# Kernel optimization log

Hardware: AMD Instinct MI355X
Metric: run time of the kernel (lower is better)

Reference implementation:

```python
import jax, jax.numpy as jnp
import numpy as np
import math

DIM_IN = 768
RED = 256
FS = 384


def setup_inputs() -> dict:
    key = jax.random.key(0)
    ks = jax.random.split(key, 20)
    B, Nq, Nk = 16, 1024, FS
    inp = {
        "query_feature": jax.random.normal(ks[0], (B, Nq, DIM_IN), jnp.float32),
        "Input_feature": jax.random.normal(ks[1], (B, Nk, DIM_IN), jnp.float32),
    }
    # six q/k projections: Linear(dim_in -> reduce_dim), torch weight layout [out,in]
    names = ["q1", "q2", "q3", "k1", "k2", "k3"]
    for i, n in enumerate(names):
        inp[f"W{n}"] = 0.01 * jax.random.normal(ks[2 + i], (RED, DIM_IN), jnp.float32)
        inp[f"b{n}"] = jnp.zeros((RED,), jnp.float32)
    # self.layer: Linear(Fs_size -> 1)
    inp["layer_w"] = 0.01 * jax.random.normal(ks[10], (1, FS), jnp.float32)
    inp["layer_b"] = jnp.zeros((1,), jnp.float32)
    # output_layer: Linear(2*dim_in -> dim_in)
    inp["Wout"] = 0.01 * jax.random.normal(ks[11], (DIM_IN, 2 * DIM_IN), jnp.float32)
    inp["bout"] = jnp.zeros((DIM_IN,), jnp.float32)
    return inp


def _proj_center(x, W, b):
    # Linear then subtract per-feature mean over the token axis (dim=1)
    y = jnp.einsum("bnd,rd->bnr", x, W) + b
    return y - y.mean(axis=1, keepdims=True)


def reference(query_feature, Input_feature,
              Wq1, bq1, Wq2, bq2, Wq3, bq3,
              Wk1, bk1, Wk2, bk2, Wk3, bk3,
              layer_w, layer_b, Wout, bout):
    scale = 1.0 / math.sqrt(RED)
    q1 = _proj_center(query_feature, Wq1, bq1)
    q2 = _proj_center(query_feature, Wq2, bq2)
    q3 = _proj_center(query_feature, Wq3, bq3)
    k1 = _proj_center(Input_feature, Wk1, bk1)
    k2 = _proj_center(Input_feature, Wk2, bk2)
    k3 = _proj_center(Input_feature, Wk3, bk3)

    aw1 = jax.nn.softmax(jnp.einsum("bnr,bmr->bnm", q1, q2) * scale, axis=2)  # [B,Nq,Nq]
    aw2 = jax.nn.softmax(jnp.einsum("bnr,bmr->bnm", k1, k2) * scale, axis=2)  # [B,Nk,Nk]
    aw3 = jax.nn.softmax(jnp.einsum("bnr,bmr->bnm", q3, k3) * scale, axis=2)  # [B,Nq,Nk]

    attention_feature1 = jnp.einsum("bnm,bmd->bnd", aw1, query_feature)  # [B,Nq,D]
    hidden = jnp.einsum("bnm,om->bno", aw2, layer_w) + layer_b  # [B,Nk,1]
    hidden = jax.nn.softmax(hidden, axis=1)
    add = aw3 + jnp.swapaxes(hidden, 1, 2)  # broadcast [B,1,Nk]
    attention_feature2 = jnp.einsum("bnm,bmd->bnd", add, Input_feature)  # [B,Nq,D]

    cat = jnp.concatenate([attention_feature1, attention_feature2], axis=2)  # [B,Nq,2D]
    out = jnp.einsum("bnc,dc->bnd", cat, Wout) + bout
    return (cat, out)
```

## Files before the change

### kernel.cpp

```cpp
#include <hip/hip_runtime.h>

#define BATCH 16
#define NQ 1024
#define NK 384
#define DIM 768
#define RED 256
#define CATD 1536

typedef __attribute__((ext_vector_type(4))) float f32x4;
typedef __attribute__((ext_vector_type(8))) short short8;

__device__ __forceinline__ short f2bf(float f) {
    unsigned u = __builtin_bit_cast(unsigned, f);
    u = (u + 0x7FFF + ((u >> 16) & 1)) >> 16;
    return (short)u;
}

#define GLOAD_LDS16(g, l) __builtin_amdgcn_global_load_lds( \
    (const __attribute__((address_space(1))) unsigned int*)(g), \
    (__attribute__((address_space(3))) unsigned int*)(l), 16, 0, 0)

struct GemmDesc {
    const short* A; const short* B;
    float* Cf; short* Cb; const float* bias;
    int K, lda, ldb, ldcf, ldcb;
    long sA, sB, sCf, sCb;
    float scale;
    int nx, ny;
    int start;
};

__global__ __launch_bounds__(256) void gemm_routed(
    GemmDesc d0, GemmDesc d1, GemmDesc d2, int nseg)
{
    __shared__ short Asl[2][128 * 64];
    __shared__ short Bsl[2][128 * 64];

    unsigned lin = blockIdx.x;
    const unsigned nwg = gridDim.x;
    const unsigned qc = nwg >> 3, rc = nwg & 7;
    const unsigned xcd = lin & 7, pos = lin >> 3;
    unsigned nid = (xcd < rc ? xcd * (qc + 1) : rc * (qc + 1) + (xcd - rc) * qc) + pos;

    GemmDesc d = d0;
    if (nseg > 1 && nid >= (unsigned)d1.start) d = d1;
    if (nseg > 2 && nid >= (unsigned)d2.start) d = d2;

    unsigned r = nid - (unsigned)d.start;
    const unsigned bx = r % (unsigned)d.nx; r /= (unsigned)d.nx;
    const unsigned by = r % (unsigned)d.ny;
    const unsigned bz = r / (unsigned)d.ny;

    const short* Ab = d.A + (long)bz * d.sA;
    const short* Bb = d.B + (long)bz * d.sB;
    const int m0 = by * 128, n0 = bx * 128;
    const int tid = threadIdx.x;
    const int lane = tid & 63, wid = tid >> 6;
    const int am0 = (wid >> 1) * 64, bn0 = (wid & 1) * 64;
    const int lr = lane & 15, lg = lane >> 4;
    const int lda = d.lda, ldb = d.ldb;

    f32x4 acc[4][4] = {};

    auto stage = [&](int buf, int k0) {
        #pragma unroll
        for (int i = 0; i < 4; i++) {
            int e = (tid + i * 256) * 8;
            int rr = e >> 6, c = e & 63;
            GLOAD_LDS16(Ab + (long)(m0 + rr) * lda + k0 + c, &Asl[buf][e]);
        }
        #pragma unroll
        for (int i = 0; i < 4; i++) {
            int e = (tid + i * 256) * 8;
            int rr = e >> 6, c = e & 63;
            GLOAD_LDS16(Bb + (long)(n0 + rr) * ldb + k0 + c, &Bsl[buf][e]);
        }
    };
    auto compute = [&](int buf) {
        #pragma unroll
        for (int ks = 0; ks < 2; ks++) {
            short8 af[4], bfv[4];
            #pragma unroll
            for (int m = 0; m < 4; m++)
                af[m] = *(const short8*)&Asl[buf][(am0 + m * 16 + lr) * 64 + ks * 32 + lg * 8];
            #pragma unroll
            for (int n = 0; n < 4; n++)
                bfv[n] = *(const short8*)&Bsl[buf][(bn0 + n * 16 + lr) * 64 + ks * 32 + lg * 8];
            #pragma unroll
            for (int m = 0; m < 4; m++)
                #pragma unroll
                for (int n = 0; n < 4; n++)
                    acc[m][n] = __builtin_amdgcn_mfma_f32_16x16x32_bf16(
                        af[m], bfv[n], acc[m][n], 0, 0, 0);
        }
    };

    const int nt = d.K >> 6;
    stage(0, 0);
    __syncthreads();
    int cur = 0;
    for (int t = 0; t < nt; ++t) {
        if (t + 1 < nt) stage(cur ^ 1, (t + 1) << 6);
        compute(cur);
        if (t + 1 < nt) { __syncthreads(); cur ^= 1; }
    }

    const float scale = d.scale;
    float* Cfb = d.Cf ? d.Cf + (long)bz * d.sCf : nullptr;
    short* Cbb = d.Cb ? d.Cb + (long)bz * d.sCb : nullptr;
    if (Cfb && Cbb) {
        #pragma unroll
        for (int m = 0; m < 4; m++)
            #pragma unroll
            for (int n = 0; n < 4; n++) {
                int col = n0 + bn0 + n * 16 + lr;
                #pragma unroll
                for (int j = 0; j < 4; j++) {
                    long row = m0 + am0 + m * 16 + lg * 4 + j;
                    float v = acc[m][n][j] * scale;
                    Cfb[row * d.ldcf + col] = v;
                    Cbb[row * d.ldcb + col] = f2bf(v);
                }
            }
    } else if (Cfb) {
        const float* bias = d.bias;
        #pragma unroll
        for (int m = 0; m < 4; m++)
            #pragma unroll
            for (int n = 0; n < 4; n++) {
                int col = n0 + bn0 + n * 16 + lr;
                float bv = bias ? bias[col] : 0.f;
                #pragma unroll
                for (int j = 0; j < 4; j++) {
                    long row = m0 + am0 + m * 16 + lg * 4 + j;
                    Cfb[row * d.ldcf + col] = acc[m][n][j] * scale + bv;
                }
            }
    } else {
        #pragma unroll
        for (int m = 0; m < 4; m++)
            #pragma unroll
            for (int n = 0; n < 4; n++) {
                int col = n0 + bn0 + n * 16 + lr;
                #pragma unroll
                for (int j = 0; j < 4; j++) {
                    long row = m0 + am0 + m * 16 + lg * 4 + j;
                    Cbb[row * d.ldcb + col] = f2bf(acc[m][n][j] * scale);
                }
            }
    }
}

__global__ __launch_bounds__(256) void colsum(
    const float* __restrict__ X, float* __restrict__ mean, int N, int chunk)
{
    int b = blockIdx.x;
    int dd = blockIdx.y * 256 + threadIdx.x;
    int n0 = blockIdx.z * chunk;
    float s = 0.f;
    for (int n = n0; n < n0 + chunk; n++)
        s += X[((long)b * N + n) * DIM + dd];
    atomicAdd(&mean[b * DIM + dd], s);
}

template<int N>
__global__ __launch_bounds__(256) void prep_input(
    const float* __restrict__ X, const float* __restrict__ mean,
    short* __restrict__ Xc, short* __restrict__ XT, float invN)
{
    __shared__ short tile[32][33];
    int b = blockIdx.z;
    int n0 = blockIdx.x * 32, d0 = blockIdx.y * 32;
    int tx = threadIdx.x & 31, ty = threadIdx.x >> 5;
    const float* Xb = X + (long)b * N * DIM;
    short* Xcb = Xc + (long)b * N * DIM;
    float mv = mean[b * DIM + d0 + tx] * invN;
    #pragma unroll
    for (int i = 0; i < 4; i++) {
        int n = n0 + ty + i * 8;
        float x = Xb[(long)n * DIM + d0 + tx];
        tile[ty + i * 8][tx] = f2bf(x);
        Xcb[(long)n * DIM + d0 + tx] = f2bf(x - mv);
    }
    __syncthreads();
    short* XTb = XT + (long)b * DIM * N;
    #pragma unroll
    for (int i = 0; i < 4; i++) {
        int dd = d0 + ty + i * 8;
        XTb[(long)dd * N + n0 + tx] = tile[tx][ty + i * 8];
    }
}

struct WP { const float* p[7]; };
__global__ __launch_bounds__(256) void cvt_weights(
    WP wp, short* __restrict__ Wqb, short* __restrict__ Wkb,
    short* __restrict__ WoutB)
{
    const int WSZ = RED * DIM / 8;
    const int OSZ = DIM * CATD / 8;
    int i = blockIdx.x * 256 + threadIdx.x;
    if (i >= 6 * WSZ + OSZ) return;
    const float* src;
    short* dst;
    if (i < 6 * WSZ) {
        int w = i / WSZ, o = i - w * WSZ;
        src = wp.p[w] + (long)o * 8;
        dst = (w < 3 ? Wqb + (long)w * RED * DIM
                     : Wkb + (long)(w - 3) * RED * DIM) + (long)o * 8;
    } else {
        int o = i - 6 * WSZ;
        src = wp.p[6] + (long)o * 8;
        dst = WoutB + (long)o * 8;
    }
    const f32x4* s = (const f32x4*)src;
    f32x4 x0 = s[0], x1 = s[1];
    short8 o8;
    o8[0] = f2bf(x0[0]); o8[1] = f2bf(x0[1]); o8[2] = f2bf(x0[2]); o8[3] = f2bf(x0[3]);
    o8[4] = f2bf(x1[0]); o8[5] = f2bf(x1[1]); o8[6] = f2bf(x1[2]); o8[7] = f2bf(x1[3]);
    *(short8*)dst = o8;
}

template<int L>
__device__ __forceinline__ void softmax_body(
    const float* __restrict__ p, short* __restrict__ po,
    const float* __restrict__ addv)
{
    const int tid = threadIdx.x;
    const int C = (L + 255) >> 8;
    float v[C];
    float mx = -3.0e38f;
    #pragma unroll
    for (int c = 0; c < C; c++) {
        int i = tid + c * 256;
        v[c] = (i < L) ? p[i] : -3.0e38f;
        mx = fmaxf(mx, v[c]);
    }
    __shared__ float rmax[4], rsum[4];
    #pragma unroll
    for (int o = 1; o < 64; o <<= 1) mx = fmaxf(mx, __shfl_xor(mx, o));
    if ((tid & 63) == 0) rmax[tid >> 6] = mx;
    __syncthreads();
    mx = fmaxf(fmaxf(rmax[0], rmax[1]), fmaxf(rmax[2], rmax[3]));
    float s = 0.f;
    #pragma unroll
    for (int c = 0; c < C; c++) {
        float e = __expf(v[c] - mx);
        v[c] = e;
        s += e;
    }
    #pragma unroll
    for (int o = 1; o < 64; o <<= 1) s += __shfl_xor(s, o);
    if ((tid & 63) == 0) rsum[tid >> 6] = s;
    __syncthreads();
    s = rsum[0] + rsum[1] + rsum[2] + rsum[3];
    float inv = 1.0f / s;
    if (addv) {
        #pragma unroll
        for (int c = 0; c < C; c++) {
            int i = tid + c * 256;
            if (i < L) po[i] = f2bf(v[c] * inv + addv[i]);
        }
    } else {
        #pragma unroll
        for (int c = 0; c < C; c++) {
            int i = tid + c * 256;
            if (i < L) po[i] = f2bf(v[c] * inv);
        }
    }
}

__global__ __launch_bounds__(256) void softmax_two(
    const float* __restrict__ S1, short* __restrict__ P1,
    const float* __restrict__ S3, short* __restrict__ P3,
    const float* __restrict__ hid)
{
    long row = blockIdx.x;
    if (row < (long)BATCH * NQ) {
        softmax_body<NQ>(S1 + row * NQ, P1 + row * NQ, nullptr);
    } else {
        row -= (long)BATCH * NQ;
        int b = (int)(row / NQ);
        softmax_body<NK>(S3 + row * NK, P3 + row * NK, hid + (long)b * NK);
    }
}

__global__ __launch_bounds__(256) void softmax_dot(
    const float* __restrict__ S2, const float* __restrict__ lw,
    float* __restrict__ scores)
{
    long row = blockIdx.x;
    const float* p = S2 + row * NK;
    const int tid = threadIdx.x;
    const int C = 2;
    float v[C];
    float mx = -3.0e38f;
    #pragma unroll
    for (int c = 0; c < C; c++) {
        int i = tid + c * 256;
        v[c] = (i < NK) ? p[i] : -3.0e38f;
        mx = fmaxf(mx, v[c]);
    }
    __shared__ float rmax[4], rsum[4], rdot[4];
    #pragma unroll
    for (int o = 1; o < 64; o <<= 1) mx = fmaxf(mx, __shfl_xor(mx, o));
    if ((tid & 63) == 0) rmax[tid >> 6] = mx;
    __syncthreads();
    mx = fmaxf(fmaxf(rmax[0], rmax[1]), fmaxf(rmax[2], rmax[3]));
    float s = 0.f, dt = 0.f;
    #pragma unroll
    for (int c = 0; c < C; c++) {
        int i = tid + c * 256;
        float e = __expf(v[c] - mx);
        s += e;
        dt += (i < NK) ? e * lw[i] : 0.f;
    }
    #pragma unroll
    for (int o = 1; o < 64; o <<= 1) { s += __shfl_xor(s, o); dt += __shfl_xor(dt, o); }
    if ((tid & 63) == 0) { rsum[tid >> 6] = s; rdot[tid >> 6] = dt; }
    __syncthreads();
    if (tid == 0) {
        s = rsum[0] + rsum[1] + rsum[2] + rsum[3];
        dt = rdot[0] + rdot[1] + rdot[2] + rdot[3];
        scores[row] = dt / s;
    }
}

__global__ __launch_bounds__(384) void hid_softmax(
    const float* __restrict__ scores, float* __restrict__ hid)
{
    int b = blockIdx.x;
    int n = threadIdx.x;
    float s = scores[b * NK + n];
    __shared__ float red[6];
    float mx = s;
    #pragma unroll
    for (int o = 1; o < 64; o <<= 1) mx = fmaxf(mx, __shfl_xor(mx, o));
    int wid = n >> 6;
    if ((n & 63) == 0) red[wid] = mx;
    __syncthreads();
    mx = red[0];
    #pragma unroll
    for (int w = 1; w < 6; w++) mx = fmaxf(mx, red[w]);
    float e = __expf(s - mx);
    float sm = e;
    #pragma unroll
    for (int o = 1; o < 64; o <<= 1) sm += __shfl_xor(sm, o);
    __syncthreads();
    if ((n & 63) == 0) red[wid] = sm;
    __syncthreads();
    sm = 0.f;
    #pragma unroll
    for (int w = 0; w < 6; w++) sm += red[w];
    hid[b * NK + n] = e / sm;
}

extern "C" void kernel_launch(void* const* d_in, const int* in_sizes, int n_in,
                              void* d_out, int out_size, void* d_ws, size_t ws_size,
                              hipStream_t stream)
{
    const float* Qf  = (const float*)d_in[0];
    const float* If  = (const float*)d_in[1];
    const float* lw  = (const float*)d_in[14];
    const float* bout= (const float*)d_in[17];

    float* cat = (float*)d_out;
    float* out = (float*)d_out + (long)BATCH * NQ * CATD;

    char* ws = (char*)d_ws;
    size_t off = 0;
    auto alloc = [&](size_t bytes) { char* p = ws + off; off += (bytes + 255) & ~(size_t)255; return p; };

    float* S1    = (float*)alloc((size_t)BATCH * NQ * NQ * 4);
    float* S2    = (float*)alloc((size_t)BATCH * NK * NK * 4);
    float* S3    = (float*)alloc((size_t)BATCH * NQ * NK * 4);
    short* Qc    = (short*)alloc((size_t)BATCH * NQ * DIM * 2);
    short* Kc    = (short*)alloc((size_t)BATCH * NK * DIM * 2);
    short* QfT   = (short*)alloc((size_t)BATCH * NQ * DIM * 2);
    short* IfT   = (short*)alloc((size_t)BATCH * NK * DIM * 2);
    short* q_all = (short*)alloc((size_t)BATCH * NQ * 3 * RED * 2);
    short* k_all = (short*)alloc((size_t)BATCH * NK * 3 * RED * 2);
    short* P1    = (short*)alloc((size_t)BATCH * NQ * NQ * 2);
    short* P3    = (short*)alloc((size_t)BATCH * NQ * NK * 2);
    short* catbf = (short*)alloc((size_t)BATCH * NQ * CATD * 2);
    short* Wqb   = (short*)alloc((size_t)3 * RED * DIM * 2);
    short* Wkb   = (short*)alloc((size_t)3 * RED * DIM * 2);
    short* WoutB = (short*)alloc((size_t)DIM * CATD * 2);
    float* means = (float*)alloc((size_t)2 * BATCH * DIM * 4);
    float* scores= (float*)alloc((size_t)BATCH * NK * 4);
    float* hid   = (float*)alloc((size_t)BATCH * NK * 4);

    float* meanQ = means;
    float* meanK = means + BATCH * DIM;

    hipMemsetAsync(means, 0, (size_t)2 * BATCH * DIM * 4, stream);

    colsum<<<dim3(BATCH, DIM / 256, NQ / 128), 256, 0, stream>>>(Qf, meanQ, NQ, 128);
    colsum<<<dim3(BATCH, DIM / 256, NK / 128), 256, 0, stream>>>(If, meanK, NK, 128);

    prep_input<NQ><<<dim3(NQ / 32, DIM / 32, BATCH), 256, 0, stream>>>(Qf, meanQ, Qc, QfT, 1.0f / NQ);
    prep_input<NK><<<dim3(NK / 32, DIM / 32, BATCH), 256, 0, stream>>>(If, meanK, Kc, IfT, 1.0f / NK);

    {
        WP wp;
        wp.p[0] = (const float*)d_in[2];
        wp.p[1] = (const float*)d_in[4];
        wp.p[2] = (const float*)d_in[6];
        wp.p[3] = (const float*)d_in[8];
        wp.p[4] = (const float*)d_in[10];
        wp.p[5] = (const float*)d_in[12];
        wp.p[6] = (const float*)d_in[16];
        int total = 6 * (RED * DIM / 8) + DIM * CATD / 8;
        cvt_weights<<<(total + 255) / 256, 256, 0, stream>>>(wp, Wqb, Wkb, WoutB);
    }

    const float scale = 0.0625f;
    const long sQ = (long)NQ * 3 * RED, sK = (long)NK * 3 * RED;
    GemmDesc z = {};

    {
        GemmDesc dq = z, dk = z;
        dq.A = Qc; dq.B = Wqb; dq.Cb = q_all;
        dq.K = DIM; dq.lda = DIM; dq.ldb = DIM; dq.ldcb = 3 * RED;
        dq.scale = 1.0f; dq.nx = 6; dq.ny = BATCH * NQ / 128; dq.start = 0;
        dk = dq; dk.A = Kc; dk.B = Wkb; dk.Cb = k_all;
        dk.ny = BATCH * NK / 128; dk.start = 6 * (BATCH * NQ / 128);
        int total = dk.start + 6 * (BATCH * NK / 128);
        gemm_routed<<<total, 256, 0, stream>>>(dq, dk, z, 2);
    }

    {
        GemmDesc a = z, b = z, c = z;
        a.A = q_all; a.B = q_all + RED; a.Cf = S1;
        a.K = RED; a.lda = 3 * RED; a.ldb = 3 * RED; a.ldcf = NQ;
        a.sA = sQ; a.sB = sQ; a.sCf = (long)NQ * NQ;
        a.scale = scale; a.nx = NQ / 128; a.ny = NQ / 128; a.start = 0;
        b.A = k_all; b.B = k_all + RED; b.Cf = S2;
        b.K = RED; b.lda = 3 * RED; b.ldb = 3 * RED; b.ldcf = NK;
        b.sA = sK; b.sB = sK; b.sCf = (long)NK * NK;
        b.scale = scale; b.nx = NK / 128; b.ny = NK / 128;
        b.start = a.nx * a.ny * BATCH;
        c.A = q_all + 2 * RED; c.B = k_all + 2 * RED; c.Cf = S3;
        c.K = RED; c.lda = 3 * RED; c.ldb = 3 * RED; c.ldcf = NK;
        c.sA = sQ; c.sB = sK; c.sCf = (long)NQ * NK;
        c.scale = scale; c.nx = NK / 128; c.ny = NQ / 128;
        c.start = b.start + b.nx * b.ny * BATCH;
        int total = c.start + c.nx * c.ny * BATCH;
        gemm_routed<<<total, 256, 0, stream>>>(a, b, c, 3);
    }

    softmax_dot<<<BATCH * NK, 256, 0, stream>>>(S2, lw, scores);
    hid_softmax<<<BATCH, NK, 0, stream>>>(scores, hid);
    softmax_two<<<2 * BATCH * NQ, 256, 0, stream>>>(S1, P1, S3, P3, hid);

    {
        GemmDesc p1 = z, p2 = z;
        p1.A = P1; p1.B = QfT; p1.Cf = cat; p1.Cb = catbf;
        p1.K = NQ; p1.lda = NQ; p1.ldb = NQ; p1.ldcf = CATD; p1.ldcb = CATD;
        p1.sA = (long)NQ * NQ; p1.sB = (long)DIM * NQ;
        p1.sCf = (long)NQ * CATD; p1.sCb = (long)NQ * CATD;
        p1.scale = 1.0f; p1.nx = DIM / 128; p1.ny = NQ / 128; p1.start = 0;
        p2 = p1;
        p2.A = P3; p2.B = IfT; p2.Cf = cat + DIM; p2.Cb = catbf + DIM;
        p2.K = NK; p2.lda = NK; p2.ldb = NK;
        p2.sA = (long)NQ * NK; p2.sB = (long)DIM * NK;
        p2.start = p1.nx * p1.ny * BATCH;
        int total = 2 * p1.nx * p1.ny * BATCH;
        gemm_routed<<<total, 256, 0, stream>>>(p1, p2, z, 2);
    }

    {
        GemmDesc f = z;
        f.A = catbf; f.B = WoutB; f.Cf = out; f.bias = bout;
        f.K = CATD; f.lda = CATD; f.ldb = CATD; f.ldcf = DIM;
        f.scale = 1.0f; f.nx = DIM / 128; f.ny = BATCH * NQ / 128; f.start = 0;
        gemm_routed<<<f.nx * f.ny, 256, 0, stream>>>(f, z, z, 1);
    }
}
```

Baseline: 666.7 us.

## Enlarge GEMM tiles to 256x256 with 512-thread blocks and bounds clamping

Replaces the 128x128-tile, 256-thread routed GEMM with a 256x256-tile, 512-thread variant in which each wave computes a 128x64 sub-tile. Row loads are clamped and stores are guarded so that dimensions like 384 that are not multiples of 256 still work. The three epilogue branches are merged into one path. The aim is more operand reuse per LDS byte and fewer workgroups. In exchange it needs 128KB of LDS per block and many more accumulator registers. Padded tiles on the 384-wide problems waste compute, and fewer, larger blocks may underfill the CUs on the small batched GEMMs.

```diff
diff --git a/kernel.cpp b/kernel.cpp
--- a/kernel.cpp
+++ b/kernel.cpp
@@ -23,18 +23,18 @@
 struct GemmDesc {
     const short* A; const short* B;
     float* Cf; short* Cb; const float* bias;
-    int K, lda, ldb, ldcf, ldcb;
+    int M, N, K, lda, ldb, ldcf, ldcb;
     long sA, sB, sCf, sCb;
     float scale;
     int nx, ny;
     int start;
 };
 
-__global__ __launch_bounds__(256) void gemm_routed(
+__global__ __launch_bounds__(512, 2) void gemm256(
     GemmDesc d0, GemmDesc d1, GemmDesc d2, int nseg)
 {
-    __shared__ short Asl[2][128 * 64];
-    __shared__ short Bsl[2][128 * 64];
+    __shared__ short Asl[2][256 * 64];
+    __shared__ short Bsl[2][256 * 64];
 
     unsigned lin = blockIdx.x;
     const unsigned nwg = gridDim.x;
@@ -53,41 +53,45 @@
 
     const short* Ab = d.A + (long)bz * d.sA;
     const short* Bb = d.B + (long)bz * d.sB;
-    const int m0 = by * 128, n0 = bx * 128;
+    const int m0 = by * 256, n0 = bx * 256;
+    const int M = d.M, N = d.N;
     const int tid = threadIdx.x;
     const int lane = tid & 63, wid = tid >> 6;
-    const int am0 = (wid >> 1) * 64, bn0 = (wid & 1) * 64;
+    const int wr = wid >> 2, wc = wid & 3;
+    const int am0 = wr * 128, bn0 = wc * 64;
     const int lr = lane & 15, lg = lane >> 4;
     const int lda = d.lda, ldb = d.ldb;
 
-    f32x4 acc[4][4] = {};
+    f32x4 acc[8][4] = {};
 
     auto stage = [&](int buf, int k0) {
         #pragma unroll
         for (int i = 0; i < 4; i++) {
-            int e = (tid + i * 256) * 8;
+            int e = (tid + i * 512) * 8;
             int rr = e >> 6, c = e & 63;
-            GLOAD_LDS16(Ab + (long)(m0 + rr) * lda + k0 + c, &Asl[buf][e]);
+            int ra = m0 + rr; if (ra > M - 1) ra = M - 1;
+            GLOAD_LDS16(Ab + (long)ra * lda + k0 + c, &Asl[buf][e]);
         }
         #pragma unroll
         for (int i = 0; i < 4; i++) {
-            int e = (tid + i * 256) * 8;
+            int e = (tid + i * 512) * 8;
             int rr = e >> 6, c = e & 63;
-            GLOAD_LDS16(Bb + (long)(n0 + rr) * ldb + k0 + c, &Bsl[buf][e]);
+            int rb = n0 + rr; if (rb > N - 1) rb = N - 1;
+            GLOAD_LDS16(Bb + (long)rb * ldb + k0 + c, &Bsl[buf][e]);
         }
     };
     auto compute = [&](int buf) {
         #pragma unroll
         for (int ks = 0; ks < 2; ks++) {
-            short8 af[4], bfv[4];
+            short8 af[8], bfv[4];
             #pragma unroll
-            for (int m = 0; m < 4; m++)
+            for (int m = 0; m < 8; m++)
                 af[m] = *(const short8*)&Asl[buf][(am0 + m * 16 + lr) * 64 + ks * 32 + lg * 8];
             #pragma unroll
             for (int n = 0; n < 4; n++)
                 bfv[n] = *(const short8*)&Bsl[buf][(bn0 + n * 16 + lr) * 64 + ks * 32 + lg * 8];
             #pragma unroll
-            for (int m = 0; m < 4; m++)
+            for (int m = 0; m < 8; m++)
                 #pragma unroll
                 for (int n = 0; n < 4; n++)
                     acc[m][n] = __builtin_amdgcn_mfma_f32_16x16x32_bf16(
@@ -102,52 +106,30 @@
     for (int t = 0; t < nt; ++t) {
         if (t + 1 < nt) stage(cur ^ 1, (t + 1) << 6);
         compute(cur);
-        if (t + 1 < nt) { __syncthreads(); cur ^= 1; }
+        __syncthreads();
+        cur ^= 1;
     }
 
     const float scale = d.scale;
     float* Cfb = d.Cf ? d.Cf + (long)bz * d.sCf : nullptr;
     short* Cbb = d.Cb ? d.Cb + (long)bz * d.sCb : nullptr;
-    if (Cfb && Cbb) {
-        #pragma unroll
-        for (int m = 0; m < 4; m++)
+    const float* bias = d.bias;
+    #pragma unroll
+    for (int m = 0; m < 8; m++) {
+        #pragma unroll
+        for (int n = 0; n < 4; n++) {
+            int col = n0 + bn0 + n * 16 + lr;
+            if (col >= N) continue;
+            float bv = bias ? bias[col] : 0.f;
             #pragma unroll
-            for (int n = 0; n < 4; n++) {
-                int col = n0 + bn0 + n * 16 + lr;
-                #pragma unroll
-                for (int j = 0; j < 4; j++) {
-                    long row = m0 + am0 + m * 16 + lg * 4 + j;
-                    float v = acc[m][n][j] * scale;
-                    Cfb[row * d.ldcf + col] = v;
-                    Cbb[row * d.ldcb + col] = f2bf(v);
-                }
+            for (int j = 0; j < 4; j++) {
+                int row = m0 + am0 + m * 16 + lg * 4 + j;
+                if (row >= M) continue;
+                float v = acc[m][n][j] * scale + bv;
+                if (Cfb) Cfb[(long)row * d.ldcf + col] = v;
+                if (Cbb) Cbb[(long)row * d.ldcb + col] = f2bf(v);
             }
-    } else if (Cfb) {
-        const float* bias = d.bias;
-        #pragma unroll
-        for (int m = 0; m < 4; m++)
-            #pragma unroll
-            for (int n = 0; n < 4; n++) {
-                int col = n0 + bn0 + n * 16 + lr;
-                float bv = bias ? bias[col] : 0.f;
-                #pragma unroll
-                for (int j = 0; j < 4; j++) {
-                    long row = m0 + am0 + m * 16 + lg * 4 + j;
-                    Cfb[row * d.ldcf + col] = acc[m][n][j] * scale + bv;
-                }
-            }
-    } else {
-        #pragma unroll
-        for (int m = 0; m < 4; m++)
-            #pragma unroll
-            for (int n = 0; n < 4; n++) {
-                int col = n0 + bn0 + n * 16 + lr;
-                #pragma unroll
-                for (int j = 0; j < 4; j++) {
-                    long row = m0 + am0 + m * 16 + lg * 4 + j;
-                    Cbb[row * d.ldcb + col] = f2bf(acc[m][n][j] * scale);
-                }
-            }
+        }
     }
 }
 
@@ -420,32 +402,37 @@
     {
         GemmDesc dq = z, dk = z;
         dq.A = Qc; dq.B = Wqb; dq.Cb = q_all;
-        dq.K = DIM; dq.lda = DIM; dq.ldb = DIM; dq.ldcb = 3 * RED;
-        dq.scale = 1.0f; dq.nx = 6; dq.ny = BATCH * NQ / 128; dq.start = 0;
+        dq.M = BATCH * NQ; dq.N = 3 * RED; dq.K = DIM;
+        dq.lda = DIM; dq.ldb = DIM; dq.ldcb = 3 * RED;
+        dq.scale = 1.0f; dq.nx = 3; dq.ny = BATCH * NQ / 256; dq.start = 0;
         dk = dq; dk.A = Kc; dk.B = Wkb; dk.Cb = k_all;
-        dk.ny = BATCH * NK / 128; dk.start = 6 * (BATCH * NQ / 128);
-        int total = dk.start + 6 * (BATCH * NK / 128);
-        gemm_routed<<<total, 256, 0, stream>>>(dq, dk, z, 2);
+        dk.M = BATCH * NK; dk.ny = BATCH * NK / 256;
+        dk.start = dq.nx * dq.ny;
+        int total = dk.start + dk.nx * dk.ny;
+        gemm256<<<total, 512, 0, stream>>>(dq, dk, z, 2);
     }
 
     {
         GemmDesc a = z, b = z, c = z;
         a.A = q_all; a.B = q_all + RED; a.Cf = S1;
-        a.K = RED; a.lda = 3 * RED; a.ldb = 3 * RED; a.ldcf = NQ;
+        a.M = NQ; a.N = NQ; a.K = RED;
+        a.lda = 3 * RED; a.ldb = 3 * RED; a.ldcf = NQ;
         a.sA = sQ; a.sB = sQ; a.sCf = (long)NQ * NQ;
-        a.scale = scale; a.nx = NQ / 128; a.ny = NQ / 128; a.start = 0;
+        a.scale = scale; a.nx = 4; a.ny = 4; a.start = 0;
         b.A = k_all; b.B = k_all + RED; b.Cf = S2;
-        b.K = RED; b.lda = 3 * RED; b.ldb = 3 * RED; b.ldcf = NK;
+        b.M = NK; b.N = NK; b.K = RED;
+        b.lda = 3 * RED; b.ldb = 3 * RED; b.ldcf = NK;
         b.sA = sK; b.sB = sK; b.sCf = (long)NK * NK;
-        b.scale = scale; b.nx = NK / 128; b.ny = NK / 128;
+        b.scale = scale; b.nx = 2; b.ny = 2;
         b.start = a.nx * a.ny * BATCH;
         c.A = q_all + 2 * RED; c.B = k_all + 2 * RED; c.Cf = S3;
-        c.K = RED; c.lda = 3 * RED; c.ldb = 3 * RED; c.ldcf = NK;
+        c.M = NQ; c.N = NK; c.K = RED;
+        c.lda = 3 * RED; c.ldb = 3 * RED; c.ldcf = NK;
         c.sA = sQ; c.sB = sK; c.sCf = (long)NQ * NK;
-        c.scale = scale; c.nx = NK / 128; c.ny = NQ / 128;
+        c.scale = scale; c.nx = 2; c.ny = 4;
         c.start = b.start + b.nx * b.ny * BATCH;
         int total = c.start + c.nx * c.ny * BATCH;
-        gemm_routed<<<total, 256, 0, stream>>>(a, b, c, 3);
+        gemm256<<<total, 512, 0, stream>>>(a, b, c, 3);
     }
 
     softmax_dot<<<BATCH * NK, 256, 0, stream>>>(S2, lw, scores);
@@ -455,24 +442,26 @@
     {
         GemmDesc p1 = z, p2 = z;
         p1.A = P1; p1.B = QfT; p1.Cf = cat; p1.Cb = catbf;
-        p1.K = NQ; p1.lda = NQ; p1.ldb = NQ; p1.ldcf = CATD; p1.ldcb = CATD;
+        p1.M = NQ; p1.N = DIM; p1.K = NQ;
+        p1.lda = NQ; p1.ldb = NQ; p1.ldcf = CATD; p1.ldcb = CATD;
         p1.sA = (long)NQ * NQ; p1.sB = (long)DIM * NQ;
         p1.sCf = (long)NQ * CATD; p1.sCb = (long)NQ * CATD;
-        p1.scale = 1.0f; p1.nx = DIM / 128; p1.ny = NQ / 128; p1.start = 0;
+        p1.scale = 1.0f; p1.nx = 3; p1.ny = 4; p1.start = 0;
         p2 = p1;
         p2.A = P3; p2.B = IfT; p2.Cf = cat + DIM; p2.Cb = catbf + DIM;
         p2.K = NK; p2.lda = NK; p2.ldb = NK;
         p2.sA = (long)NQ * NK; p2.sB = (long)DIM * NK;
         p2.start = p1.nx * p1.ny * BATCH;
         int total = 2 * p1.nx * p1.ny * BATCH;
-        gemm_routed<<<total, 256, 0, stream>>>(p1, p2, z, 2);
+        gemm256<<<total, 512, 0, stream>>>(p1, p2, z, 2);
     }
 
     {
         GemmDesc f = z;
         f.A = catbf; f.B = WoutB; f.Cf = out; f.bias = bout;
-        f.K = CATD; f.lda = CATD; f.ldb = CATD; f.ldcf = DIM;
-        f.scale = 1.0f; f.nx = DIM / 128; f.ny = BATCH * NQ / 128; f.start = 0;
-        gemm_routed<<<f.nx * f.ny, 256, 0, stream>>>(f, z, z, 1);
-    }
-}
+        f.M = BATCH * NQ; f.N = DIM; f.K = CATD;
+        f.lda = CATD; f.ldb = CATD; f.ldcf = DIM;
+        f.scale = 1.0f; f.nx = 3; f.ny = BATCH * NQ / 256; f.start = 0;
+        gemm256<<<f.nx * f.ny, 512, 0, stream>>>(f, z, z, 1);
+    }
+}
```

Result: slower. 760.3 us (+14.0%).

## Store attention scores as bf16 in place and single-buffer GEMM LDS

Applied to the files above, without the earlier changes.

Attention score matrices S1/S2/S3 are now written by the GEMM as bf16 rather than fp32. The softmax kernels read them as bf16 and overwrite them in place, which removes the separate P1/P3 buffers and halves score-matrix traffic. The GEMM also drops LDS double buffering for a single buffer with two barriers per k-step. That halves shared memory per block, which may raise occupancy, but it gives up overlap between loads and MFMA work. Rounding the scores to bf16 before softmax also loses some precision.

```diff
diff --git a/kernel.cpp b/kernel.cpp
--- a/kernel.cpp
+++ b/kernel.cpp
@@ -14,6 +14,10 @@
     unsigned u = __builtin_bit_cast(unsigned, f);
     u = (u + 0x7FFF + ((u >> 16) & 1)) >> 16;
     return (short)u;
+}
+__device__ __forceinline__ float bf2f(short s) {
+    unsigned u = ((unsigned)(unsigned short)s) << 16;
+    return __builtin_bit_cast(float, u);
 }
 
 #define GLOAD_LDS16(g, l) __builtin_amdgcn_global_load_lds( \
@@ -33,8 +37,8 @@
 __global__ __launch_bounds__(256) void gemm_routed(
     GemmDesc d0, GemmDesc d1, GemmDesc d2, int nseg)
 {
-    __shared__ short Asl[2][128 * 64];
-    __shared__ short Bsl[2][128 * 64];
+    __shared__ short Asl[128 * 64];
+    __shared__ short Bsl[128 * 64];
 
     unsigned lin = blockIdx.x;
     const unsigned nwg = gridDim.x;
@@ -62,30 +66,29 @@
 
     f32x4 acc[4][4] = {};
 
-    auto stage = [&](int buf, int k0) {
+    for (int k0 = 0; k0 < d.K; k0 += 64) {
         #pragma unroll
         for (int i = 0; i < 4; i++) {
             int e = (tid + i * 256) * 8;
             int rr = e >> 6, c = e & 63;
-            GLOAD_LDS16(Ab + (long)(m0 + rr) * lda + k0 + c, &Asl[buf][e]);
+            GLOAD_LDS16(Ab + (long)(m0 + rr) * lda + k0 + c, Asl + e);
         }
         #pragma unroll
         for (int i = 0; i < 4; i++) {
             int e = (tid + i * 256) * 8;
             int rr = e >> 6, c = e & 63;
-            GLOAD_LDS16(Bb + (long)(n0 + rr) * ldb + k0 + c, &Bsl[buf][e]);
+            GLOAD_LDS16(Bb + (long)(n0 + rr) * ldb + k0 + c, Bsl + e);
         }
-    };
-    auto compute = [&](int buf) {
+        __syncthreads();
         #pragma unroll
         for (int ks = 0; ks < 2; ks++) {
             short8 af[4], bfv[4];
             #pragma unroll
             for (int m = 0; m < 4; m++)
-                af[m] = *(const short8*)&Asl[buf][(am0 + m * 16 + lr) * 64 + ks * 32 + lg * 8];
+                af[m] = *(const short8*)&Asl[(am0 + m * 16 + lr) * 64 + ks * 32 + lg * 8];
             #pragma unroll
             for (int n = 0; n < 4; n++)
-                bfv[n] = *(const short8*)&Bsl[buf][(bn0 + n * 16 + lr) * 64 + ks * 32 + lg * 8];
+                bfv[n] = *(const short8*)&Bsl[(bn0 + n * 16 + lr) * 64 + ks * 32 + lg * 8];
             #pragma unroll
             for (int m = 0; m < 4; m++)
                 #pragma unroll
@@ -93,16 +96,7 @@
                     acc[m][n] = __builtin_amdgcn_mfma_f32_16x16x32_bf16(
                         af[m], bfv[n], acc[m][n], 0, 0, 0);
         }
-    };
-
-    const int nt = d.K >> 6;
-    stage(0, 0);
-    __syncthreads();
-    int cur = 0;
-    for (int t = 0; t < nt; ++t) {
-        if (t + 1 < nt) stage(cur ^ 1, (t + 1) << 6);
-        compute(cur);
-        if (t + 1 < nt) { __syncthreads(); cur ^= 1; }
+        __syncthreads();
     }
 
     const float scale = d.scale;
@@ -222,8 +216,7 @@
 
 template<int L>
 __device__ __forceinline__ void softmax_body(
-    const float* __restrict__ p, short* __restrict__ po,
-    const float* __restrict__ addv)
+    short* __restrict__ p, const float* __restrict__ addv)
 {
     const int tid = threadIdx.x;
     const int C = (L + 255) >> 8;
@@ -232,7 +225,7 @@
     #pragma unroll
     for (int c = 0; c < C; c++) {
         int i = tid + c * 256;
-        v[c] = (i < L) ? p[i] : -3.0e38f;
+        v[c] = (i < L) ? bf2f(p[i]) : -3.0e38f;
         mx = fmaxf(mx, v[c]);
     }
     __shared__ float rmax[4], rsum[4];
@@ -258,46 +251,44 @@
         #pragma unroll
         for (int c = 0; c < C; c++) {
             int i = tid + c * 256;
-            if (i < L) po[i] = f2bf(v[c] * inv + addv[i]);
+            if (i < L) p[i] = f2bf(v[c] * inv + addv[i]);
         }
     } else {
         #pragma unroll
         for (int c = 0; c < C; c++) {
             int i = tid + c * 256;
-            if (i < L) po[i] = f2bf(v[c] * inv);
+            if (i < L) p[i] = f2bf(v[c] * inv);
         }
     }
 }
 
 __global__ __launch_bounds__(256) void softmax_two(
-    const float* __restrict__ S1, short* __restrict__ P1,
-    const float* __restrict__ S3, short* __restrict__ P3,
+    short* __restrict__ S1, short* __restrict__ S3,
     const float* __restrict__ hid)
 {
     long row = blockIdx.x;
     if (row < (long)BATCH * NQ) {
-        softmax_body<NQ>(S1 + row * NQ, P1 + row * NQ, nullptr);
+        softmax_body<NQ>(S1 + row * NQ, nullptr);
     } else {
         row -= (long)BATCH * NQ;
         int b = (int)(row / NQ);
-        softmax_body<NK>(S3 + row * NK, P3 + row * NK, hid + (long)b * NK);
+        softmax_body<NK>(S3 + row * NK, hid + (long)b * NK);
     }
 }
 
 __global__ __launch_bounds__(256) void softmax_dot(
-    const float* __restrict__ S2, const float* __restrict__ lw,
+    const short* __restrict__ S2, const float* __restrict__ lw,
     float* __restrict__ scores)
 {
     long row = blockIdx.x;
-    const float* p = S2 + row * NK;
+    const short* p = S2 + row * NK;
     const int tid = threadIdx.x;
-    const int C = 2;
-    float v[C];
+    float v[2];
     float mx = -3.0e38f;
     #pragma unroll
-    for (int c = 0; c < C; c++) {
+    for (int c = 0; c < 2; c++) {
         int i = tid + c * 256;
-        v[c] = (i < NK) ? p[i] : -3.0e38f;
+        v[c] = (i < NK) ? bf2f(p[i]) : -3.0e38f;
         mx = fmaxf(mx, v[c]);
     }
     __shared__ float rmax[4], rsum[4], rdot[4];
@@ -308,7 +299,7 @@
     mx = fmaxf(fmaxf(rmax[0], rmax[1]), fmaxf(rmax[2], rmax[3]));
     float s = 0.f, dt = 0.f;
     #pragma unroll
-    for (int c = 0; c < C; c++) {
+    for (int c = 0; c < 2; c++) {
         int i = tid + c * 256;
         float e = __expf(v[c] - mx);
         s += e;
@@ -370,17 +361,15 @@
     size_t off = 0;
     auto alloc = [&](size_t bytes) { char* p = ws + off; off += (bytes + 255) & ~(size_t)255; return p; };
 
-    float* S1    = (float*)alloc((size_t)BATCH * NQ * NQ * 4);
-    float* S2    = (float*)alloc((size_t)BATCH * NK * NK * 4);
-    float* S3    = (float*)alloc((size_t)BATCH * NQ * NK * 4);
+    short* S1    = (short*)alloc((size_t)BATCH * NQ * NQ * 2);
+    short* S2    = (short*)alloc((size_t)BATCH * NK * NK * 2);
+    short* S3    = (short*)alloc((size_t)BATCH * NQ * NK * 2);
     short* Qc    = (short*)alloc((size_t)BATCH * NQ * DIM * 2);
     short* Kc    = (short*)alloc((size_t)BATCH * NK * DIM * 2);
     short* QfT   = (short*)alloc((size_t)BATCH * NQ * DIM * 2);
     short* IfT   = (short*)alloc((size_t)BATCH * NK * DIM * 2);
     short* q_all = (short*)alloc((size_t)BATCH * NQ * 3 * RED * 2);
     short* k_all = (short*)alloc((size_t)BATCH * NK * 3 * RED * 2);
-    short* P1    = (short*)alloc((size_t)BATCH * NQ * NQ * 2);
-    short* P3    = (short*)alloc((size_t)BATCH * NQ * NK * 2);
     short* catbf = (short*)alloc((size_t)BATCH * NQ * CATD * 2);
     short* Wqb   = (short*)alloc((size_t)3 * RED * DIM * 2);
     short* Wkb   = (short*)alloc((size_t)3 * RED * DIM * 2);
@@ -430,18 +419,18 @@
 
     {
         GemmDesc a = z, b = z, c = z;
-        a.A = q_all; a.B = q_all + RED; a.Cf = S1;
-        a.K = RED; a.lda = 3 * RED; a.ldb = 3 * RED; a.ldcf = NQ;
-        a.sA = sQ; a.sB = sQ; a.sCf = (long)NQ * NQ;
+        a.A = q_all; a.B = q_all + RED; a.Cb = S1;
+        a.K = RED; a.lda = 3 * RED; a.ldb = 3 * RED; a.ldcb = NQ;
+        a.sA = sQ; a.sB = sQ; a.sCb = (long)NQ * NQ;
         a.scale = scale; a.nx = NQ / 128; a.ny = NQ / 128; a.start = 0;
-        b.A = k_all; b.B = k_all + RED; b.Cf = S2;
-        b.K = RED; b.lda = 3 * RED; b.ldb = 3 * RED; b.ldcf = NK;
-        b.sA = sK; b.sB = sK; b.sCf = (long)NK * NK;
+        b.A = k_all; b.B = k_all + RED; b.Cb = S2;
+        b.K = RED; b.lda = 3 * RED; b.ldb = 3 * RED; b.ldcb = NK;
+        b.sA = sK; b.sB = sK; b.sCb = (long)NK * NK;
         b.scale = scale; b.nx = NK / 128; b.ny = NK / 128;
         b.start = a.nx * a.ny * BATCH;
-        c.A = q_all + 2 * RED; c.B = k_all + 2 * RED; c.Cf = S3;
-        c.K = RED; c.lda = 3 * RED; c.ldb = 3 * RED; c.ldcf = NK;
-        c.sA = sQ; c.sB = sK; c.sCf = (long)NQ * NK;
+        c.A = q_all + 2 * RED; c.B = k_all + 2 * RED; c.Cb = S3;
+        c.K = RED; c.lda = 3 * RED; c.ldb = 3 * RED; c.ldcb = NK;
+        c.sA = sQ; c.sB = sK; c.sCb = (long)NQ * NK;
         c.scale = scale; c.nx = NK / 128; c.ny = NQ / 128;
         c.start = b.start + b.nx * b.ny * BATCH;
         int total = c.start + c.nx * c.ny * BATCH;
@@ -450,17 +439,17 @@
 
     softmax_dot<<<BATCH * NK, 256, 0, stream>>>(S2, lw, scores);
     hid_softmax<<<BATCH, NK, 0, stream>>>(scores, hid);
-    softmax_two<<<2 * BATCH * NQ, 256, 0, stream>>>(S1, P1, S3, P3, hid);
+    softmax_two<<<2 * BATCH * NQ, 256, 0, stream>>>(S1, S3, hid);
 
     {
         GemmDesc p1 = z, p2 = z;
-        p1.A = P1; p1.B = QfT; p1.Cf = cat; p1.Cb = catbf;
+        p1.A = S1; p1.B = QfT; p1.Cf = cat; p1.Cb = catbf;
         p1.K = NQ; p1.lda = NQ; p1.ldb = NQ; p1.ldcf = CATD; p1.ldcb = CATD;
         p1.sA = (long)NQ * NQ; p1.sB = (long)DIM * NQ;
         p1.sCf = (long)NQ * CATD; p1.sCb = (long)NQ * CATD;
         p1.scale = 1.0f; p1.nx = DIM / 128; p1.ny = NQ / 128; p1.start = 0;
         p2 = p1;
-        p2.A = P3; p2.B = IfT; p2.Cf = cat + DIM; p2.Cb = catbf + DIM;
+        p2.A = S3; p2.B = IfT; p2.Cf = cat + DIM; p2.Cb = catbf + DIM;
         p2.K = NK; p2.lda = NK; p2.ldb = NK;
         p2.sA = (long)NQ * NK; p2.sB = (long)DIM * NK;
         p2.start = p1.nx * p1.ny * BATCH;
```

New measurement: 649.0 us. 1.03x faster.
